# Kernel optimization log

Measured on AMD Instinct MI355X. Metric: run time of the kernel, lower is better.

## Reference

```python
import jax, jax.numpy as jnp
import numpy as np

MODES = 16
WIDTH = 64
INPUT_DIM = 12
N_LAYERS = 4
FACTOR = 2
B, M, N = 16, 128, 128


def _ff(x, w1, b1, w2, b2):
    # FeedForward: Linear -> ReLU -> Linear
    return jax.nn.relu(x @ w1 + b1) @ w2 + b2


def setup_inputs() -> dict:
    key = jax.random.key(0)
    ks = jax.random.split(key, 24)
    D, H = WIDTH, WIDTH * FACTOR
    # xavier-ish scale for complex fourier weights: sqrt(2/(fan_in+fan_out))
    fw_scale = float(np.sqrt(2.0 / (D + D)))
    def rn(k, shape, s=0.05):
        return (jax.random.normal(k, shape, dtype=jnp.float32) * s)
    return {
        "x": jax.random.normal(ks[0], (B, M, N, INPUT_DIM), dtype=jnp.float32),
        "in_w": rn(ks[1], (INPUT_DIM, D), 0.2),
        "in_b": jnp.zeros((D,), jnp.float32),
        "fwy_re": rn(ks[2], (N_LAYERS, D, D, MODES), fw_scale),
        "fwy_im": rn(ks[3], (N_LAYERS, D, D, MODES), fw_scale),
        "fwx_re": rn(ks[4], (N_LAYERS, D, D, MODES), fw_scale),
        "fwx_im": rn(ks[5], (N_LAYERS, D, D, MODES), fw_scale),
        "bc_w1": rn(ks[6], (N_LAYERS, D, H), 0.1),
        "bc_b1": jnp.zeros((N_LAYERS, H), jnp.float32),
        "bc_w2": rn(ks[7], (N_LAYERS, H, D), 0.1),
        "bc_b2": jnp.zeros((N_LAYERS, D), jnp.float32),
        "fc_w1": rn(ks[8], (N_LAYERS, D, H), 0.1),
        "fc_b1": jnp.zeros((N_LAYERS, H), jnp.float32),
        "fc_w2": rn(ks[9], (N_LAYERS, H, D), 0.1),
        "fc_b2": jnp.zeros((N_LAYERS, D), jnp.float32),
        "out_w1": rn(ks[10], (D, 128), 0.1),
        "out_b1": jnp.zeros((128,), jnp.float32),
        "out_w2": rn(ks[11], (128, 1), 0.1),
        "out_b2": jnp.zeros((1,), jnp.float32),
    }


def reference(x, in_w, in_b, fwy_re, fwy_im, fwx_re, fwx_im,
              bc_w1, bc_b1, bc_w2, bc_b2, fc_w1, fc_b1, fc_w2, fc_b2,
              out_w1, out_b1, out_w2, out_b2):
    fwy = (fwy_re + 1j * fwy_im).astype(jnp.complex64)  # [L, I, O, modes]
    fwx = (fwx_re + 1j * fwx_im).astype(jnp.complex64)
    x = x @ in_w + in_b  # [B, M, N, width]
    forecast = jnp.zeros(x.shape[:3] + (1,), x.dtype)
    for i in range(N_LAYERS):
        xt = jnp.transpose(x, (0, 3, 1, 2))  # b i m n
        _, _, Mm, Nn = xt.shape
        # spectral conv along last (y) axis
        fty = jnp.fft.rfft(xt, axis=-1, norm='ortho')  # [B,I,M,N//2+1]
        py = jnp.einsum('bixy,ioy->boxy', fty[..., :MODES], fwy[i])
        py = jnp.pad(py, ((0, 0), (0, 0), (0, 0), (0, Nn // 2 + 1 - MODES)))
        xy = jnp.fft.irfft(py, n=Nn, axis=-1, norm='ortho')
        # spectral conv along second-to-last (x) axis
        ftx = jnp.fft.rfft(xt, axis=-2, norm='ortho')  # [B,I,M//2+1,N]
        px = jnp.einsum('bixy,iox->boxy', ftx[:, :, :MODES, :], fwx[i])
        px = jnp.pad(px, ((0, 0), (0, 0), (0, Mm // 2 + 1 - MODES), (0, 0)))
        xx = jnp.fft.irfft(px, n=Mm, axis=-2, norm='ortho')
        xs = jnp.transpose(xx + xy, (0, 2, 3, 1))  # b m n i
        b = _ff(xs, bc_w1[i], bc_b1[i], bc_w2[i], bc_b2[i])
        f = _ff(xs, fc_w1[i], fc_b1[i], fc_w2[i], fc_b2[i])
        f_out = (f @ out_w1 + out_b1) @ out_w2 + out_b2  # [B,M,N,1]
        forecast = forecast + f_out
        x = x - b  # next_input='subtract'
    return forecast
```

## Files before the change

kernel.cpp:

```cpp
#include <hip/hip_runtime.h>

#define B_    16
#define M_    128
#define N_    128
#define DIN   12
#define D_    64
#define H_    128
#define MODES 16
#define NL    4
#define NPIX  262144

typedef float  f32x2 __attribute__((ext_vector_type(2)));
typedef float  f32x4 __attribute__((ext_vector_type(4)));
typedef short  s16x8 __attribute__((ext_vector_type(8)));
typedef unsigned int u32x4 __attribute__((ext_vector_type(4)));

#define WSB_X      0L
#define WSB_XSX    67108864L
#define WSB_BF     100663296L
#define WSB_BI     100671488L
#define WSB_U      100679680L
#define WSB_D      100681728L
#define WSB_WFF    100681744L
#define WSB_WMIX   100878352L
#define WS_NEEDED  102975504L

__device__ __forceinline__ unsigned short f2bf(float f){
    unsigned int u = __float_as_uint(f);
    u += 0x7fffu + ((u >> 16) & 1u);
    return (unsigned short)(u >> 16);
}
__device__ __forceinline__ float bf2f(unsigned short s){
    return __uint_as_float(((unsigned int)s) << 16);
}

__global__ void k_init(const float* __restrict__ out_w1, const float* __restrict__ out_b1,
                       const float* __restrict__ out_w2, const float* __restrict__ out_b2,
                       const float* __restrict__ fc_w2, const float* __restrict__ fc_b2,
                       float* __restrict__ ws){
    __shared__ float v_s[64];
    __shared__ float c_s;
    int t = threadIdx.x;
    if (t < 64){
        float a = 0.f;
        for (int j = 0; j < H_; j++) a += out_w1[t*H_ + j] * out_w2[j];
        v_s[t] = a;
    }
    if (t == 64){
        float a = 0.f;
        for (int j = 0; j < H_; j++) a += out_b1[j] * out_w2[j];
        c_s = a + out_b2[0];
    }
    __syncthreads();
    float* uw = (float*)((char*)ws + WSB_U);
    float* dw = (float*)((char*)ws + WSB_D);
    if (t < 128){
        for (int l = 0; l < NL; l++){
            float a = 0.f;
            for (int o = 0; o < D_; o++) a += fc_w2[(l*H_ + t)*D_ + o] * v_s[o];
            uw[l*128 + t] = a;
        }
    }
    if (t >= 128 && t < 132){
        int l = t - 128;
        float a = 0.f;
        for (int o = 0; o < D_; o++) a += fc_b2[l*D_ + o] * v_s[o];
        dw[l] = a + c_s;
    }
    const float isn = 0.08838834764831845f;
    unsigned short* bft = (unsigned short*)((char*)ws + WSB_BF);
    unsigned short* bit = (unsigned short*)((char*)ws + WSB_BI);
    for (int e = t; e < 4096; e += 256){
        { int kp = e >> 7, n = e & 127, k = kp >> 1;
          float ang = 6.283185307179586f * (float)((k*n) & 127) / 128.0f;
          bft[e] = f2bf((kp & 1) ? (-sinf(ang)*isn) : (cosf(ang)*isn)); }
        { int n = e >> 5, kp = e & 31, k = kp >> 1;
          float ang = 6.283185307179586f * (float)((k*n) & 127) / 128.0f;
          float val;
          if (kp & 1) val = (k == 0) ? 0.f : (-2.f*sinf(ang)*isn);
          else        val = ((k == 0) ? 1.f : 2.f) * cosf(ang) * isn;
          bit[e] = f2bf(val); }
    }
}

__global__ void k_wconv(const float* __restrict__ bc_w1, const float* __restrict__ fc_w1,
                        const float* __restrict__ bc_w2, float* __restrict__ ws){
    unsigned short* wb = (unsigned short*)((char*)ws + WSB_WFF);
    int e = blockIdx.x*256 + threadIdx.x;
    int a = e >> 15;
    int r = e & 32767;
    int l = r >> 13;
    int q = r & 8191;
    if (a == 0){
        int j = q >> 6, i = q & 63;
        wb[e] = f2bf(bc_w1[(l*D_ + i)*H_ + j]);
    } else if (a == 1){
        int j = q >> 6, i = q & 63;
        wb[e] = f2bf(fc_w1[(l*D_ + i)*H_ + j]);
    } else {
        int o = q >> 7, j = q & 127;
        wb[e] = f2bf(bc_w2[(l*H_ + j)*D_ + o]);
    }
}

__global__ void k_wmix(const float* __restrict__ fwy_re, const float* __restrict__ fwy_im,
                       const float* __restrict__ fwx_re, const float* __restrict__ fwx_im,
                       float* __restrict__ ws){
    unsigned int* wm = (unsigned int*)((char*)ws + WSB_WMIX);
    int e = blockIdx.x*256 + threadIdx.x;
    int ax = e >> 18;
    int r  = e & 262143;
    int l  = r >> 16;
    int k  = (r >> 12) & 15;
    int i  = (r >> 6) & 63;
    int o  = r & 63;
    long sidx = (((long)l*64 + i)*64 + o)*16 + k;
    float re = ax ? fwx_re[sidx] : fwy_re[sidx];
    float im = ax ? fwx_im[sidx] : fwy_im[sidx];
    wm[e] = (unsigned int)f2bf(re) | ((unsigned int)f2bf(im) << 16);
}

__global__ __launch_bounds__(256) void k_embed(const float* __restrict__ xin,
                                               const float* __restrict__ in_w,
                                               const float* __restrict__ in_b,
                                               float* __restrict__ X){
    long row = (long)blockIdx.x*4 + (threadIdx.x >> 6);
    int d = threadIdx.x & 63;
    const float* xr = xin + row*DIN;
    float acc = in_b[d];
    #pragma unroll
    for (int i = 0; i < DIN; i++) acc += xr[i] * in_w[i*D_ + d];
    X[row*D_ + d] = acc;
}

__global__ __launch_bounds__(256, 3) void k_spec_x(float* __restrict__ ws_f, int layer){
    __shared__ __attribute__((aligned(16))) char lds[49152];
    int t = threadIdx.x, w = t >> 6, lane = t & 63;
    int l15 = lane & 15, l4 = lane >> 4;
    int bb = blockIdx.x >> 6;
    int c  = blockIdx.x & 63;
    const float* X = ws_f;

    for (int s = 0; s < 2; s++){
        long base = (long)bb*1048576 + (long)(c*2 + s)*64;
        char* xst = lds + s*16384;
        #pragma unroll
        for (int it = 0; it < 4; it++){
            int iq = t & 15, np = (t >> 4) + it*16;
            int i0 = iq*4;
            f32x4 v0 = *(const f32x4*)&X[base + (long)(2*np)*8192 + i0];
            f32x4 v1 = *(const f32x4*)&X[base + (long)(2*np + 1)*8192 + i0];
            #pragma unroll
            for (int j = 0; j < 4; j++){
                int i = i0 + j;
                unsigned int pk = (unsigned int)f2bf(v0[j]) | ((unsigned int)f2bf(v1[j]) << 16);
                *(unsigned int*)(xst + i*256 + ((np*4) ^ ((i & 15) << 4))) = pk;
            }
        }
    }
    {
        const unsigned short* bfg = (const unsigned short*)((char*)ws_f + WSB_BF);
        for (int e = t; e < 512; e += 256){
            int kp = e >> 4, c16 = e & 15;
            s16x8 v = *(const s16x8*)&bfg[e*8];
            *(s16x8*)(lds + 32768 + kp*256 + ((c16*16) ^ ((kp & 7) << 4))) = v;
        }
    }
    __syncthreads();

    int mt = w & 1, nt0 = (w >> 1)*2;
    for (int s = 0; s < 2; s++){
        char* xst = lds + s*16384;
        f32x4 acc[2] = {{0.f,0.f,0.f,0.f},{0.f,0.f,0.f,0.f}};
        #pragma unroll
        for (int ks = 0; ks < 4; ks++){
            int kpr = mt*16 + l15;
            s16x8 a = *(const s16x8*)(lds + 32768 + kpr*256 + (((l4*16) + ks*64) ^ ((kpr & 7) << 4)));
            #pragma unroll
            for (int nf = 0; nf < 2; nf++){
                int i = (nt0 + nf)*16 + l15;
                s16x8 b = *(const s16x8*)(xst + i*256 + (((l4*16) + ks*64) ^ ((i & 15) << 4)));
                acc[nf] = __builtin_amdgcn_mfma_f32_16x16x32_bf16(a, b, acc[nf], 0, 0, 0);
            }
        }
        char* Ts = lds + 40960 + s*4096;
        #pragma unroll
        for (int nf = 0; nf < 2; nf++){
            int i = (nt0 + nf)*16 + l15;
            #pragma unroll
            for (int q = 0; q < 4; q++){
                int kp = mt*16 + l4*4 + q;
                *(unsigned short*)(Ts + kp*128 + ((i*2) ^ ((kp & 7) << 4))) = f2bf(acc[nf][q]);
            }
        }
    }
    __syncthreads();

    {
        const unsigned short* big = (const unsigned short*)((char*)ws_f + WSB_BI);
        for (int e = t; e < 512; e += 256){
            int n = e >> 2, k8 = e & 3;
            s16x8 v = *(const s16x8*)&big[e*8];
            *(s16x8*)(lds + n*80 + ((k8*16) ^ ((n & 3) << 4))) = v;
        }
    }
    {
        int k = t >> 4, og = t & 15;
        const unsigned int* Wg = (const unsigned int*)((char*)ws_f + WSB_WMIX)
                                 + ((long)(4 + layer)*16 + k)*4096;
        const char* T0 = lds + 40960;
        const char* T1 = lds + 45056;
        int rre = 2*k, rim = 2*k + 1;
        float pre0[4] = {0,0,0,0}, pim0[4] = {0,0,0,0};
        float pre1[4] = {0,0,0,0}, pim1[4] = {0,0,0,0};
        for (int i0 = 0; i0 < 64; i0 += 8){
            s16x8 tr0 = *(const s16x8*)(T0 + rre*128 + ((i0*2) ^ ((rre & 7) << 4)));
            s16x8 ti0 = *(const s16x8*)(T0 + rim*128 + ((i0*2) ^ ((rim & 7) << 4)));
            s16x8 tr1 = *(const s16x8*)(T1 + rre*128 + ((i0*2) ^ ((rre & 7) << 4)));
            s16x8 ti1 = *(const s16x8*)(T1 + rim*128 + ((i0*2) ^ ((rim & 7) << 4)));
            #pragma unroll
            for (int e = 0; e < 8; e++){
                u32x4 wv = *(const u32x4*)&Wg[(i0 + e)*64 + og*4];
                float a0 = bf2f((unsigned short)tr0[e]), b0 = bf2f((unsigned short)ti0[e]);
                float a1 = bf2f((unsigned short)tr1[e]), b1 = bf2f((unsigned short)ti1[e]);
                #pragma unroll
                for (int j = 0; j < 4; j++){
                    float wre = bf2f((unsigned short)(wv[j] & 0xffffu));
                    float wim = bf2f((unsigned short)(wv[j] >> 16));
                    pre0[j] += a0*wre - b0*wim;  pim0[j] += a0*wim + b0*wre;
                    pre1[j] += a1*wre - b1*wim;  pim1[j] += a1*wim + b1*wre;
                }
            }
        }
        #pragma unroll
        for (int j = 0; j < 4; j++){
            int o = og*4 + j;
            unsigned int pk0 = (unsigned int)f2bf(pre0[j]) | ((unsigned int)f2bf(pim0[j]) << 16);
            unsigned int pk1 = (unsigned int)f2bf(pre1[j]) | ((unsigned int)f2bf(pim1[j]) << 16);
            *(unsigned int*)(lds + 10240 + o*80 + ((k*4) ^ ((o & 3) << 4))) = pk0;
            *(unsigned int*)(lds + 15360 + o*80 + ((k*4) ^ ((o & 3) << 4))) = pk1;
        }
    }
    __syncthreads();

    unsigned short* XSx = (unsigned short*)((char*)ws_f + WSB_XSX);
    for (int s = 0; s < 2; s++){
        const char* Ps = lds + 10240 + s*5120;
        int nc = c*2 + s;
        s16x8 bfr[4];
        #pragma unroll
        for (int nt = 0; nt < 4; nt++){
            int o = nt*16 + l15;
            bfr[nt] = *(const s16x8*)(Ps + o*80 + ((l4*16) ^ ((o & 3) << 4)));
        }
        f32x4 acc[2][4];
        #pragma unroll
        for (int mi = 0; mi < 2; mi++){
            int n_ = (w*2 + mi)*16 + l15;
            s16x8 a = *(const s16x8*)(lds + n_*80 + ((l4*16) ^ ((n_ & 3) << 4)));
            #pragma unroll
            for (int nt = 0; nt < 4; nt++){
                f32x4 z = {0.f,0.f,0.f,0.f};
                acc[mi][nt] = __builtin_amdgcn_mfma_f32_16x16x32_bf16(a, bfr[nt], z, 0, 0, 0);
            }
        }
        #pragma unroll
        for (int mi = 0; mi < 2; mi++)
        #pragma unroll
        for (int nt = 0; nt < 4; nt++)
        #pragma unroll
        for (int q = 0; q < 4; q++){
            int m = (w*2 + mi)*16 + l4*4 + q;
            int o = nt*16 + l15;
            XSx[(long)bb*1048576 + (long)m*8192 + nc*64 + o] = f2bf(acc[mi][nt][q]);
        }
    }
}

__global__ __launch_bounds__(256, 2) void k_spec_y_ff(
        float* __restrict__ ws_f, float* __restrict__ out,
        const float* __restrict__ bc_b1, const float* __restrict__ bc_b2,
        const float* __restrict__ fc_b1, int layer, int first){
    __shared__ __attribute__((aligned(16))) char lds[65536];
    int t = threadIdx.x, w = t >> 6, lane = t & 63;
    int l15 = lane & 15, l4 = lane >> 4;
    long slab = blockIdx.x;
    float* X = ws_f;
    long xbase = slab*8192;

    #pragma unroll
    for (int it = 0; it < 4; it++){
        int iq = t & 15, np = (t >> 4) + it*16;
        int i0 = iq*4;
        f32x4 v0 = *(const f32x4*)&X[xbase + (long)(2*np)*64 + i0];
        f32x4 v1 = *(const f32x4*)&X[xbase + (long)(2*np + 1)*64 + i0];
        #pragma unroll
        for (int j = 0; j < 4; j++){
            int i = i0 + j;
            unsigned int pk = (unsigned int)f2bf(v0[j]) | ((unsigned int)f2bf(v1[j]) << 16);
            *(unsigned int*)(lds + i*256 + ((np*4) ^ ((i & 15) << 4))) = pk;
        }
    }
    {
        const unsigned short* bfg = (const unsigned short*)((char*)ws_f + WSB_BF);
        for (int e = t; e < 512; e += 256){
            int kp = e >> 4, c16 = e & 15;
            s16x8 v = *(const s16x8*)&bfg[e*8];
            *(s16x8*)(lds + 16384 + kp*256 + ((c16*16) ^ ((kp & 7) << 4))) = v;
        }
        const unsigned short* big = (const unsigned short*)((char*)ws_f + WSB_BI);
        for (int e = t; e < 512; e += 256){
            int n = e >> 2, k8 = e & 3;
            s16x8 v = *(const s16x8*)&big[e*8];
            *(s16x8*)(lds + 36864 + n*80 + ((k8*16) ^ ((n & 3) << 4))) = v;
        }
    }
    __syncthreads();

    {
        int mt = w & 1, nt0 = (w >> 1)*2;
        f32x4 acc[2] = {{0.f,0.f,0.f,0.f},{0.f,0.f,0.f,0.f}};
        #pragma unroll
        for (int ks = 0; ks < 4; ks++){
            int kpr = mt*16 + l15;
            s16x8 a = *(const s16x8*)(lds + 16384 + kpr*256 + (((l4*16) + ks*64) ^ ((kpr & 7) << 4)));
            #pragma unroll
            for (int nf = 0; nf < 2; nf++){
                int i = (nt0 + nf)*16 + l15;
                s16x8 b = *(const s16x8*)(lds + i*256 + (((l4*16) + ks*64) ^ ((i & 15) << 4)));
                acc[nf] = __builtin_amdgcn_mfma_f32_16x16x32_bf16(a, b, acc[nf], 0, 0, 0);
            }
        }
        #pragma unroll
        for (int nf = 0; nf < 2; nf++){
            int i = (nt0 + nf)*16 + l15;
            #pragma unroll
            for (int q = 0; q < 4; q++){
                int kp = mt*16 + l4*4 + q;
                *(unsigned short*)(lds + 32768 + kp*128 + ((i*2) ^ ((kp & 7) << 4))) = f2bf(acc[nf][q]);
            }
        }
    }
    __syncthreads();

    {
        int k = t >> 4, og = t & 15;
        const unsigned int* Wg = (const unsigned int*)((char*)ws_f + WSB_WMIX)
                                 + ((long)layer*16 + k)*4096;
        const char* T0 = lds + 32768;
        int rre = 2*k, rim = 2*k + 1;
        float pre[4] = {0,0,0,0}, pim[4] = {0,0,0,0};
        for (int i0 = 0; i0 < 64; i0 += 8){
            s16x8 tr = *(const s16x8*)(T0 + rre*128 + ((i0*2) ^ ((rre & 7) << 4)));
            s16x8 ti = *(const s16x8*)(T0 + rim*128 + ((i0*2) ^ ((rim & 7) << 4)));
            #pragma unroll
            for (int e = 0; e < 8; e++){
                u32x4 wv = *(const u32x4*)&Wg[(i0 + e)*64 + og*4];
                float a0 = bf2f((unsigned short)tr[e]), b0 = bf2f((unsigned short)ti[e]);
                #pragma unroll
                for (int j = 0; j < 4; j++){
                    float wre = bf2f((unsigned short)(wv[j] & 0xffffu));
                    float wim = bf2f((unsigned short)(wv[j] >> 16));
                    pre[j] += a0*wre - b0*wim;
                    pim[j] += a0*wim + b0*wre;
                }
            }
        }
        #pragma unroll
        for (int j = 0; j < 4; j++){
            int o = og*4 + j;
            unsigned int pk = (unsigned int)f2bf(pre[j]) | ((unsigned int)f2bf(pim[j]) << 16);
            *(unsigned int*)(lds + 47104 + o*80 + ((k*4) ^ ((o & 3) << 4))) = pk;
        }
    }
    __syncthreads();

    {
        const unsigned short* XSxg = (const unsigned short*)((char*)ws_f + WSB_XSX) + slab*8192;
        s16x8 bfr[4];
        #pragma unroll
        for (int nt = 0; nt < 4; nt++){
            int o = nt*16 + l15;
            bfr[nt] = *(const s16x8*)(lds + 47104 + o*80 + ((l4*16) ^ ((o & 3) << 4)));
        }
        f32x4 acc[2][4];
        #pragma unroll
        for (int mi = 0; mi < 2; mi++){
            int n_ = (w*2 + mi)*16 + l15;
            s16x8 a = *(const s16x8*)(lds + 36864 + n_*80 + ((l4*16) ^ ((n_ & 3) << 4)));
            #pragma unroll
            for (int nt = 0; nt < 4; nt++){
                f32x4 z = {0.f,0.f,0.f,0.f};
                acc[mi][nt] = __builtin_amdgcn_mfma_f32_16x16x32_bf16(a, bfr[nt], z, 0, 0, 0);
            }
        }
        #pragma unroll
        for (int mi = 0; mi < 2; mi++)
        #pragma unroll
        for (int nt = 0; nt < 4; nt++)
        #pragma unroll
        for (int q = 0; q < 4; q++){
            int n_ = (w*2 + mi)*16 + l4*4 + q;
            int o = nt*16 + l15;
            float v = acc[mi][nt][q] + bf2f(XSxg[n_*64 + o]);
            *(unsigned short*)(lds + n_*128 + ((o*2) ^ ((n_ & 7) << 4))) = f2bf(v);
        }
    }
    const unsigned short* wb = (const unsigned short*)((char*)ws_f + WSB_WFF);
    {
        const u32x4* src = (const u32x4*)(wb + (long)layer*8192);
        for (int cq = t; cq < 1024; cq += 256){
            int r = cq >> 3, c8 = cq & 7;
            *(u32x4*)(lds + 16384 + r*128 + ((c8 << 4) ^ ((r & 7) << 4))) = src[cq];
        }
    }
    __syncthreads();

    {
        f32x4 acc[2][8];
        #pragma unroll
        for (int mi = 0; mi < 2; mi++)
        #pragma unroll
        for (int nf = 0; nf < 8; nf++) acc[mi][nf] = (f32x4){0.f,0.f,0.f,0.f};
        #pragma unroll
        for (int ks = 0; ks < 2; ks++){
            int kch = l4 + ks*4;
            int r0 = w*32 + l15, r1 = w*32 + 16 + l15;
            s16x8 a0 = *(const s16x8*)(lds + r0*128 + ((kch << 4) ^ ((r0 & 7) << 4)));
            s16x8 a1 = *(const s16x8*)(lds + r1*128 + ((kch << 4) ^ ((r1 & 7) << 4)));
            #pragma unroll
            for (int nf = 0; nf < 8; nf++){
                int n = nf*16 + l15;
                s16x8 b = *(const s16x8*)(lds + 16384 + n*128 + ((kch << 4) ^ ((n & 7) << 4)));
                acc[0][nf] = __builtin_amdgcn_mfma_f32_16x16x32_bf16(a0, b, acc[0][nf], 0, 0, 0);
                acc[1][nf] = __builtin_amdgcn_mfma_f32_16x16x32_bf16(a1, b, acc[1][nf], 0, 0, 0);
            }
        }
        #pragma unroll
        for (int mi = 0; mi < 2; mi++)
        #pragma unroll
        for (int nf = 0; nf < 8; nf++){
            int ncol = nf*16 + l15;
            float b1 = bc_b1[layer*128 + ncol];
            #pragma unroll
            for (int q = 0; q < 4; q++){
                int mrow = w*32 + mi*16 + l4*4 + q;
                float hv = fmaxf(acc[mi][nf][q] + b1, 0.f);
                *(unsigned short*)(lds + 32768 + mrow*256 + (((ncol >> 3) << 4) ^ ((mrow & 7) << 4)) + (ncol & 7)*2) = f2bf(hv);
            }
        }
    }
    __syncthreads();
    {
        const u32x4* src = (const u32x4*)(wb + 65536 + (long)layer*8192);
        for (int cq = t; cq < 1024; cq += 256){
            int r = cq >> 4, c16 = cq & 15;
            *(u32x4*)(lds + 16384 + r*256 + ((c16 << 4) ^ ((r & 7) << 4))) = src[cq];
        }
    }
    __syncthreads();
    {
        f32x4 acc[2][4];
        #pragma unroll
        for (int mi = 0; mi < 2; mi++)
        #pragma unroll
        for (int nf = 0; nf < 4; nf++) acc[mi][nf] = (f32x4){0.f,0.f,0.f,0.f};
        #pragma unroll
        for (int ks = 0; ks < 4; ks++){
            int kch = l4 + ks*4;
            int r0 = w*32 + l15, r1 = w*32 + 16 + l15;
            s16x8 a0 = *(const s16x8*)(lds + 32768 + r0*256 + ((kch << 4) ^ ((r0 & 7) << 4)));
            s16x8 a1 = *(const s16x8*)(lds + 32768 + r1*256 + ((kch << 4) ^ ((r1 & 7) << 4)));
            #pragma unroll
            for (int nf = 0; nf < 4; nf++){
                int n = nf*16 + l15;
                s16x8 b = *(const s16x8*)(lds + 16384 + n*256 + ((kch << 4) ^ ((n & 7) << 4)));
                acc[0][nf] = __builtin_amdgcn_mfma_f32_16x16x32_bf16(a0, b, acc[0][nf], 0, 0, 0);
                acc[1][nf] = __builtin_amdgcn_mfma_f32_16x16x32_bf16(a1, b, acc[1][nf], 0, 0, 0);
            }
        }
        #pragma unroll
        for (int mi = 0; mi < 2; mi++)
        #pragma unroll
        for (int nf = 0; nf < 4; nf++){
            int ncol = nf*16 + l15;
            float b2 = bc_b2[layer*64 + ncol];
            #pragma unroll
            for (int q = 0; q < 4; q++){
                int mrow = w*32 + mi*16 + l4*4 + q;
                long g = xbase + (long)mrow*64 + ncol;
                X[g] = X[g] - (acc[mi][nf][q] + b2);
            }
        }
    }
    __syncthreads();
    {
        const u32x4* src = (const u32x4*)(wb + 32768 + (long)layer*8192);
        for (int cq = t; cq < 1024; cq += 256){
            int r = cq >> 3, c8 = cq & 7;
            *(u32x4*)(lds + 16384 + r*128 + ((c8 << 4) ^ ((r & 7) << 4))) = src[cq];
        }
    }
    __syncthreads();
    {
        f32x4 acc[2][8];
        #pragma unroll
        for (int mi = 0; mi < 2; mi++)
        #pragma unroll
        for (int nf = 0; nf < 8; nf++) acc[mi][nf] = (f32x4){0.f,0.f,0.f,0.f};
        #pragma unroll
        for (int ks = 0; ks < 2; ks++){
            int kch = l4 + ks*4;
            int r0 = w*32 + l15, r1 = w*32 + 16 + l15;
            s16x8 a0 = *(const s16x8*)(lds + r0*128 + ((kch << 4) ^ ((r0 & 7) << 4)));
            s16x8 a1 = *(const s16x8*)(lds + r1*128 + ((kch << 4) ^ ((r1 & 7) << 4)));
            #pragma unroll
            for (int nf = 0; nf < 8; nf++){
                int n = nf*16 + l15;
                s16x8 b = *(const s16x8*)(lds + 16384 + n*128 + ((kch << 4) ^ ((n & 7) << 4)));
                acc[0][nf] = __builtin_amdgcn_mfma_f32_16x16x32_bf16(a0, b, acc[0][nf], 0, 0, 0);
                acc[1][nf] = __builtin_amdgcn_mfma_f32_16x16x32_bf16(a1, b, acc[1][nf], 0, 0, 0);
            }
        }
        #pragma unroll
        for (int mi = 0; mi < 2; mi++)
        #pragma unroll
        for (int nf = 0; nf < 8; nf++){
            int ncol = nf*16 + l15;
            float b1 = fc_b1[layer*128 + ncol];
            #pragma unroll
            for (int q = 0; q < 4; q++){
                int mrow = w*32 + mi*16 + l4*4 + q;
                float hv = fmaxf(acc[mi][nf][q] + b1, 0.f);
                *(unsigned short*)(lds + 32768 + mrow*256 + (((ncol >> 3) << 4) ^ ((mrow & 7) << 4)) + (ncol & 7)*2) = f2bf(hv);
            }
        }
    }
    __syncthreads();
    {
        int r = t >> 1, half = t & 1;
        const float* up = (const float*)((char*)ws_f + WSB_U) + layer*128 + half*64;
        float sum = 0.f;
        #pragma unroll
        for (int c = 0; c < 8; c++){
            int kch = half*8 + c;
            s16x8 hv = *(const s16x8*)(lds + 32768 + r*256 + ((kch << 4) ^ ((r & 7) << 4)));
            #pragma unroll
            for (int e = 0; e < 8; e++) sum += bf2f((unsigned short)hv[e]) * up[c*8 + e];
        }
        sum += __shfl_xor(sum, 1);
        if (half == 0){
            float fo = sum + *((const float*)((char*)ws_f + WSB_D) + layer);
            long g = slab*128 + r;
            if (first) out[g] = fo; else out[g] += fo;
        }
    }
}

extern "C" void kernel_launch(void* const* d_in, const int* in_sizes, int n_in,
                              void* d_out, int out_size, void* d_ws, size_t ws_size,
                              hipStream_t stream){
    if (ws_size < (size_t)WS_NEEDED) return;
    const float* xin    = (const float*)d_in[0];
    const float* in_w   = (const float*)d_in[1];
    const float* in_b   = (const float*)d_in[2];
    const float* fwy_re = (const float*)d_in[3];
    const float* fwy_im = (const float*)d_in[4];
    const float* fwx_re = (const float*)d_in[5];
    const float* fwx_im = (const float*)d_in[6];
    const float* bc_w1  = (const float*)d_in[7];
    const float* bc_b1  = (const float*)d_in[8];
    const float* bc_w2  = (const float*)d_in[9];
    const float* bc_b2  = (const float*)d_in[10];
    const float* fc_w1  = (const float*)d_in[11];
    const float* fc_b1  = (const float*)d_in[12];
    const float* fc_w2  = (const float*)d_in[13];
    const float* fc_b2  = (const float*)d_in[14];
    const float* out_w1 = (const float*)d_in[15];
    const float* out_b1 = (const float*)d_in[16];
    const float* out_w2 = (const float*)d_in[17];
    const float* out_b2 = (const float*)d_in[18];
    float* ws  = (float*)d_ws;
    float* out = (float*)d_out;

    k_init<<<1, 256, 0, stream>>>(out_w1, out_b1, out_w2, out_b2, fc_w2, fc_b2, ws);
    k_wconv<<<384, 256, 0, stream>>>(bc_w1, fc_w1, bc_w2, ws);
    k_wmix<<<2048, 256, 0, stream>>>(fwy_re, fwy_im, fwx_re, fwx_im, ws);
    k_embed<<<NPIX/4, 256, 0, stream>>>(xin, in_w, in_b, ws);

    for (int l = 0; l < NL; l++){
        k_spec_x<<<1024, 256, 0, stream>>>(ws, l);
        k_spec_y_ff<<<2048, 256, 0, stream>>>(ws, out, bc_b1, bc_b2, fc_b1, l, l == 0 ? 1 : 0);
    }
}
```

Before: 620.2 us.

## Cut LDS footprint, keep small DFT matrices in registers, fuse final projection reduction

Both spectral kernels now load the forward and inverse DFT basis fragments straight from global memory into registers instead of staging them in LDS. The LDS buffers are reused and shrunk so more blocks fit per CU, and launch bounds are raised to match. Other changes: a packed bf16 convert instruction replaces manual rounding, the complex mode mixing is vectorized into float2 operations, and the y-FF activation fragments are kept in registers. The last fc hidden layer is reduced against the projection vector directly from MFMA accumulators with lane shuffles, removing an LDS round trip and a barrier. The trade-offs are extra global loads of small matrices, more register pressure against the higher occupancy target, and rounding that differs slightly through the packed convert.

```diff
diff --git a/kernel.cpp b/kernel.cpp
--- a/kernel.cpp
+++ b/kernel.cpp
@@ -32,6 +32,11 @@
 }
 __device__ __forceinline__ float bf2f(unsigned short s){
     return __uint_as_float(((unsigned int)s) << 16);
+}
+__device__ __forceinline__ unsigned int cvtpk(float lo, float hi){
+    unsigned int r;
+    asm("v_cvt_pk_bf16_f32 %0, %1, %2" : "=v"(r) : "v"(lo), "v"(hi));
+    return r;
 }
 
 __global__ void k_init(const float* __restrict__ out_w1, const float* __restrict__ out_b1,
@@ -133,8 +138,8 @@
     X[row*D_ + d] = acc;
 }
 
-__global__ __launch_bounds__(256, 3) void k_spec_x(float* __restrict__ ws_f, int layer){
-    __shared__ __attribute__((aligned(16))) char lds[49152];
+__global__ __launch_bounds__(256, 4) void k_spec_x(float* __restrict__ ws_f, int layer){
+    __shared__ __attribute__((aligned(16))) char lds[40960];
     int t = threadIdx.x, w = t >> 6, lane = t & 63;
     int l15 = lane & 15, l4 = lane >> 4;
     int bb = blockIdx.x >> 6;
@@ -153,66 +158,56 @@
             #pragma unroll
             for (int j = 0; j < 4; j++){
                 int i = i0 + j;
-                unsigned int pk = (unsigned int)f2bf(v0[j]) | ((unsigned int)f2bf(v1[j]) << 16);
-                *(unsigned int*)(xst + i*256 + ((np*4) ^ ((i & 15) << 4))) = pk;
-            }
-        }
-    }
+                *(unsigned int*)(xst + i*256 + ((np*4) ^ ((i & 15) << 4))) = cvtpk(v0[j], v1[j]);
+            }
+        }
+    }
+    __syncthreads();
+
+    int mt = w & 1, nt0 = (w >> 1)*2;
     {
         const unsigned short* bfg = (const unsigned short*)((char*)ws_f + WSB_BF);
-        for (int e = t; e < 512; e += 256){
-            int kp = e >> 4, c16 = e & 15;
-            s16x8 v = *(const s16x8*)&bfg[e*8];
-            *(s16x8*)(lds + 32768 + kp*256 + ((c16*16) ^ ((kp & 7) << 4))) = v;
-        }
-    }
-    __syncthreads();
-
-    int mt = w & 1, nt0 = (w >> 1)*2;
-    for (int s = 0; s < 2; s++){
-        char* xst = lds + s*16384;
-        f32x4 acc[2] = {{0.f,0.f,0.f,0.f},{0.f,0.f,0.f,0.f}};
-        #pragma unroll
-        for (int ks = 0; ks < 4; ks++){
-            int kpr = mt*16 + l15;
-            s16x8 a = *(const s16x8*)(lds + 32768 + kpr*256 + (((l4*16) + ks*64) ^ ((kpr & 7) << 4)));
+        int kpr = mt*16 + l15;
+        s16x8 bfA[4];
+        #pragma unroll
+        for (int ks = 0; ks < 4; ks++)
+            bfA[ks] = *(const s16x8*)&bfg[kpr*128 + (l4 + ks*4)*8];
+        for (int s = 0; s < 2; s++){
+            char* xst = lds + s*16384;
+            f32x4 acc[2] = {{0.f,0.f,0.f,0.f},{0.f,0.f,0.f,0.f}};
+            #pragma unroll
+            for (int ks = 0; ks < 4; ks++){
+                #pragma unroll
+                for (int nf = 0; nf < 2; nf++){
+                    int i = (nt0 + nf)*16 + l15;
+                    s16x8 b = *(const s16x8*)(xst + i*256 + (((l4*16) + ks*64) ^ ((i & 15) << 4)));
+                    acc[nf] = __builtin_amdgcn_mfma_f32_16x16x32_bf16(bfA[ks], b, acc[nf], 0, 0, 0);
+                }
+            }
+            char* Ts = lds + 32768 + s*4096;
             #pragma unroll
             for (int nf = 0; nf < 2; nf++){
                 int i = (nt0 + nf)*16 + l15;
-                s16x8 b = *(const s16x8*)(xst + i*256 + (((l4*16) + ks*64) ^ ((i & 15) << 4)));
-                acc[nf] = __builtin_amdgcn_mfma_f32_16x16x32_bf16(a, b, acc[nf], 0, 0, 0);
-            }
-        }
-        char* Ts = lds + 40960 + s*4096;
-        #pragma unroll
-        for (int nf = 0; nf < 2; nf++){
-            int i = (nt0 + nf)*16 + l15;
-            #pragma unroll
-            for (int q = 0; q < 4; q++){
-                int kp = mt*16 + l4*4 + q;
-                *(unsigned short*)(Ts + kp*128 + ((i*2) ^ ((kp & 7) << 4))) = f2bf(acc[nf][q]);
-            }
-        }
-    }
-    __syncthreads();
-
-    {
-        const unsigned short* big = (const unsigned short*)((char*)ws_f + WSB_BI);
-        for (int e = t; e < 512; e += 256){
-            int n = e >> 2, k8 = e & 3;
-            s16x8 v = *(const s16x8*)&big[e*8];
-            *(s16x8*)(lds + n*80 + ((k8*16) ^ ((n & 3) << 4))) = v;
-        }
-    }
+                #pragma unroll
+                for (int q = 0; q < 4; q++){
+                    int kp = mt*16 + l4*4 + q;
+                    *(unsigned short*)(Ts + kp*128 + ((i*2) ^ ((kp & 7) << 4))) = f2bf(acc[nf][q]);
+                }
+            }
+        }
+    }
+    __syncthreads();
+
     {
         int k = t >> 4, og = t & 15;
         const unsigned int* Wg = (const unsigned int*)((char*)ws_f + WSB_WMIX)
                                  + ((long)(4 + layer)*16 + k)*4096;
-        const char* T0 = lds + 40960;
-        const char* T1 = lds + 45056;
+        const char* T0 = lds + 32768;
+        const char* T1 = lds + 36864;
         int rre = 2*k, rim = 2*k + 1;
-        float pre0[4] = {0,0,0,0}, pim0[4] = {0,0,0,0};
-        float pre1[4] = {0,0,0,0}, pim1[4] = {0,0,0,0};
+        f32x2 p0[4], p1[4];
+        #pragma unroll
+        for (int j = 0; j < 4; j++){ p0[j] = (f32x2){0.f,0.f}; p1[j] = (f32x2){0.f,0.f}; }
         for (int i0 = 0; i0 < 64; i0 += 8){
             s16x8 tr0 = *(const s16x8*)(T0 + rre*128 + ((i0*2) ^ ((rre & 7) << 4)));
             s16x8 ti0 = *(const s16x8*)(T0 + rim*128 + ((i0*2) ^ ((rim & 7) << 4)));
@@ -221,72 +216,77 @@
             #pragma unroll
             for (int e = 0; e < 8; e++){
                 u32x4 wv = *(const u32x4*)&Wg[(i0 + e)*64 + og*4];
-                float a0 = bf2f((unsigned short)tr0[e]), b0 = bf2f((unsigned short)ti0[e]);
-                float a1 = bf2f((unsigned short)tr1[e]), b1 = bf2f((unsigned short)ti1[e]);
+                f32x2 a0 = {bf2f((unsigned short)tr0[e]), bf2f((unsigned short)tr0[e])};
+                f32x2 b0 = {bf2f((unsigned short)ti0[e]), bf2f((unsigned short)ti0[e])};
+                f32x2 a1 = {bf2f((unsigned short)tr1[e]), bf2f((unsigned short)tr1[e])};
+                f32x2 b1 = {bf2f((unsigned short)ti1[e]), bf2f((unsigned short)ti1[e])};
                 #pragma unroll
                 for (int j = 0; j < 4; j++){
-                    float wre = bf2f((unsigned short)(wv[j] & 0xffffu));
-                    float wim = bf2f((unsigned short)(wv[j] >> 16));
-                    pre0[j] += a0*wre - b0*wim;  pim0[j] += a0*wim + b0*wre;
-                    pre1[j] += a1*wre - b1*wim;  pim1[j] += a1*wim + b1*wre;
+                    float wre = __uint_as_float(wv[j] << 16);
+                    float wim = __uint_as_float(wv[j] & 0xffff0000u);
+                    f32x2 w1v = {wre, wim};
+                    f32x2 w2v = {-wim, wre};
+                    p0[j] += a0*w1v + b0*w2v;
+                    p1[j] += a1*w1v + b1*w2v;
                 }
             }
         }
         #pragma unroll
         for (int j = 0; j < 4; j++){
             int o = og*4 + j;
-            unsigned int pk0 = (unsigned int)f2bf(pre0[j]) | ((unsigned int)f2bf(pim0[j]) << 16);
-            unsigned int pk1 = (unsigned int)f2bf(pre1[j]) | ((unsigned int)f2bf(pim1[j]) << 16);
-            *(unsigned int*)(lds + 10240 + o*80 + ((k*4) ^ ((o & 3) << 4))) = pk0;
-            *(unsigned int*)(lds + 15360 + o*80 + ((k*4) ^ ((o & 3) << 4))) = pk1;
+            *(unsigned int*)(lds + o*80 + ((k*4) ^ ((o & 3) << 4)))        = cvtpk(p0[j][0], p0[j][1]);
+            *(unsigned int*)(lds + 5120 + o*80 + ((k*4) ^ ((o & 3) << 4))) = cvtpk(p1[j][0], p1[j][1]);
         }
     }
     __syncthreads();
 
     unsigned short* XSx = (unsigned short*)((char*)ws_f + WSB_XSX);
-    for (int s = 0; s < 2; s++){
-        const char* Ps = lds + 10240 + s*5120;
-        int nc = c*2 + s;
-        s16x8 bfr[4];
-        #pragma unroll
-        for (int nt = 0; nt < 4; nt++){
-            int o = nt*16 + l15;
-            bfr[nt] = *(const s16x8*)(Ps + o*80 + ((l4*16) ^ ((o & 3) << 4)));
-        }
-        f32x4 acc[2][4];
+    {
+        const unsigned short* big = (const unsigned short*)((char*)ws_f + WSB_BI);
+        s16x8 aInv[2];
         #pragma unroll
         for (int mi = 0; mi < 2; mi++){
             int n_ = (w*2 + mi)*16 + l15;
-            s16x8 a = *(const s16x8*)(lds + n_*80 + ((l4*16) ^ ((n_ & 3) << 4)));
+            aInv[mi] = *(const s16x8*)&big[n_*32 + l4*8];
+        }
+        for (int s = 0; s < 2; s++){
+            const char* Ps = lds + s*5120;
+            int nc = c*2 + s;
+            s16x8 bfr[4];
             #pragma unroll
             for (int nt = 0; nt < 4; nt++){
-                f32x4 z = {0.f,0.f,0.f,0.f};
-                acc[mi][nt] = __builtin_amdgcn_mfma_f32_16x16x32_bf16(a, bfr[nt], z, 0, 0, 0);
-            }
-        }
-        #pragma unroll
-        for (int mi = 0; mi < 2; mi++)
-        #pragma unroll
-        for (int nt = 0; nt < 4; nt++)
-        #pragma unroll
-        for (int q = 0; q < 4; q++){
-            int m = (w*2 + mi)*16 + l4*4 + q;
-            int o = nt*16 + l15;
-            XSx[(long)bb*1048576 + (long)m*8192 + nc*64 + o] = f2bf(acc[mi][nt][q]);
-        }
-    }
-}
-
-__global__ __launch_bounds__(256, 2) void k_spec_y_ff(
+                int o = nt*16 + l15;
+                bfr[nt] = *(const s16x8*)(Ps + o*80 + ((l4*16) ^ ((o & 3) << 4)));
+            }
+            #pragma unroll
+            for (int mi = 0; mi < 2; mi++){
+                #pragma unroll
+                for (int nt = 0; nt < 4; nt++){
+                    f32x4 z = {0.f,0.f,0.f,0.f};
+                    f32x4 acc = __builtin_amdgcn_mfma_f32_16x16x32_bf16(aInv[mi], bfr[nt], z, 0, 0, 0);
+                    #pragma unroll
+                    for (int q = 0; q < 4; q++){
+                        int m = (w*2 + mi)*16 + l4*4 + q;
+                        int o = nt*16 + l15;
+                        XSx[(long)bb*1048576 + (long)m*8192 + nc*64 + o] = f2bf(acc[q]);
+                    }
+                }
+            }
+        }
+    }
+}
+
+__global__ __launch_bounds__(256, 3) void k_spec_y_ff(
         float* __restrict__ ws_f, float* __restrict__ out,
         const float* __restrict__ bc_b1, const float* __restrict__ bc_b2,
         const float* __restrict__ fc_b1, int layer, int first){
-    __shared__ __attribute__((aligned(16))) char lds[65536];
+    __shared__ __attribute__((aligned(16))) char lds[49152];
     int t = threadIdx.x, w = t >> 6, lane = t & 63;
     int l15 = lane & 15, l4 = lane >> 4;
     long slab = blockIdx.x;
     float* X = ws_f;
     long xbase = slab*8192;
+    const unsigned short* wb = (const unsigned short*)((char*)ws_f + WSB_WFF);
 
     #pragma unroll
     for (int it = 0; it < 4; it++){
@@ -297,33 +297,19 @@
         #pragma unroll
         for (int j = 0; j < 4; j++){
             int i = i0 + j;
-            unsigned int pk = (unsigned int)f2bf(v0[j]) | ((unsigned int)f2bf(v1[j]) << 16);
-            *(unsigned int*)(lds + i*256 + ((np*4) ^ ((i & 15) << 4))) = pk;
-        }
-    }
+            *(unsigned int*)(lds + i*256 + ((np*4) ^ ((i & 15) << 4))) = cvtpk(v0[j], v1[j]);
+        }
+    }
+    __syncthreads();
+
+    int mt = w & 1, nt0 = (w >> 1)*2;
     {
         const unsigned short* bfg = (const unsigned short*)((char*)ws_f + WSB_BF);
-        for (int e = t; e < 512; e += 256){
-            int kp = e >> 4, c16 = e & 15;
-            s16x8 v = *(const s16x8*)&bfg[e*8];
-            *(s16x8*)(lds + 16384 + kp*256 + ((c16*16) ^ ((kp & 7) << 4))) = v;
-        }
-        const unsigned short* big = (const unsigned short*)((char*)ws_f + WSB_BI);
-        for (int e = t; e < 512; e += 256){
-            int n = e >> 2, k8 = e & 3;
-            s16x8 v = *(const s16x8*)&big[e*8];
-            *(s16x8*)(lds + 36864 + n*80 + ((k8*16) ^ ((n & 3) << 4))) = v;
-        }
-    }
-    __syncthreads();
-
-    {
-        int mt = w & 1, nt0 = (w >> 1)*2;
+        int kpr = mt*16 + l15;
         f32x4 acc[2] = {{0.f,0.f,0.f,0.f},{0.f,0.f,0.f,0.f}};
         #pragma unroll
         for (int ks = 0; ks < 4; ks++){
-            int kpr = mt*16 + l15;
-            s16x8 a = *(const s16x8*)(lds + 16384 + kpr*256 + (((l4*16) + ks*64) ^ ((kpr & 7) << 4)));
+            s16x8 a = *(const s16x8*)&bfg[kpr*128 + (l4 + ks*4)*8];
             #pragma unroll
             for (int nf = 0; nf < 2; nf++){
                 int i = (nt0 + nf)*16 + l15;
@@ -337,7 +323,7 @@
             #pragma unroll
             for (int q = 0; q < 4; q++){
                 int kp = mt*16 + l4*4 + q;
-                *(unsigned short*)(lds + 32768 + kp*128 + ((i*2) ^ ((kp & 7) << 4))) = f2bf(acc[nf][q]);
+                *(unsigned short*)(lds + 16384 + kp*128 + ((i*2) ^ ((kp & 7) << 4))) = f2bf(acc[nf][q]);
             }
         }
     }
@@ -347,71 +333,79 @@
         int k = t >> 4, og = t & 15;
         const unsigned int* Wg = (const unsigned int*)((char*)ws_f + WSB_WMIX)
                                  + ((long)layer*16 + k)*4096;
-        const char* T0 = lds + 32768;
+        const char* T0 = lds + 16384;
         int rre = 2*k, rim = 2*k + 1;
-        float pre[4] = {0,0,0,0}, pim[4] = {0,0,0,0};
+        f32x2 p[4];
+        #pragma unroll
+        for (int j = 0; j < 4; j++) p[j] = (f32x2){0.f,0.f};
         for (int i0 = 0; i0 < 64; i0 += 8){
             s16x8 tr = *(const s16x8*)(T0 + rre*128 + ((i0*2) ^ ((rre & 7) << 4)));
             s16x8 ti = *(const s16x8*)(T0 + rim*128 + ((i0*2) ^ ((rim & 7) << 4)));
             #pragma unroll
             for (int e = 0; e < 8; e++){
                 u32x4 wv = *(const u32x4*)&Wg[(i0 + e)*64 + og*4];
-                float a0 = bf2f((unsigned short)tr[e]), b0 = bf2f((unsigned short)ti[e]);
+                f32x2 av = {bf2f((unsigned short)tr[e]), bf2f((unsigned short)tr[e])};
+                f32x2 bv = {bf2f((unsigned short)ti[e]), bf2f((unsigned short)ti[e])};
                 #pragma unroll
                 for (int j = 0; j < 4; j++){
-                    float wre = bf2f((unsigned short)(wv[j] & 0xffffu));
-                    float wim = bf2f((unsigned short)(wv[j] >> 16));
-                    pre[j] += a0*wre - b0*wim;
-                    pim[j] += a0*wim + b0*wre;
+                    float wre = __uint_as_float(wv[j] << 16);
+                    float wim = __uint_as_float(wv[j] & 0xffff0000u);
+                    f32x2 w1v = {wre, wim};
+                    f32x2 w2v = {-wim, wre};
+                    p[j] += av*w1v + bv*w2v;
                 }
             }
         }
         #pragma unroll
         for (int j = 0; j < 4; j++){
             int o = og*4 + j;
-            unsigned int pk = (unsigned int)f2bf(pre[j]) | ((unsigned int)f2bf(pim[j]) << 16);
-            *(unsigned int*)(lds + 47104 + o*80 + ((k*4) ^ ((o & 3) << 4))) = pk;
-        }
-    }
-    __syncthreads();
-
-    {
+            *(unsigned int*)(lds + 20480 + o*80 + ((k*4) ^ ((o & 3) << 4))) = cvtpk(p[j][0], p[j][1]);
+        }
+    }
+    __syncthreads();
+
+    {
+        const unsigned short* big = (const unsigned short*)((char*)ws_f + WSB_BI);
         const unsigned short* XSxg = (const unsigned short*)((char*)ws_f + WSB_XSX) + slab*8192;
         s16x8 bfr[4];
         #pragma unroll
         for (int nt = 0; nt < 4; nt++){
             int o = nt*16 + l15;
-            bfr[nt] = *(const s16x8*)(lds + 47104 + o*80 + ((l4*16) ^ ((o & 3) << 4)));
-        }
-        f32x4 acc[2][4];
+            bfr[nt] = *(const s16x8*)(lds + 20480 + o*80 + ((l4*16) ^ ((o & 3) << 4)));
+        }
         #pragma unroll
         for (int mi = 0; mi < 2; mi++){
             int n_ = (w*2 + mi)*16 + l15;
-            s16x8 a = *(const s16x8*)(lds + 36864 + n_*80 + ((l4*16) ^ ((n_ & 3) << 4)));
+            s16x8 a = *(const s16x8*)&big[n_*32 + l4*8];
             #pragma unroll
             for (int nt = 0; nt < 4; nt++){
                 f32x4 z = {0.f,0.f,0.f,0.f};
-                acc[mi][nt] = __builtin_amdgcn_mfma_f32_16x16x32_bf16(a, bfr[nt], z, 0, 0, 0);
-            }
-        }
-        #pragma unroll
-        for (int mi = 0; mi < 2; mi++)
-        #pragma unroll
-        for (int nt = 0; nt < 4; nt++)
-        #pragma unroll
-        for (int q = 0; q < 4; q++){
-            int n_ = (w*2 + mi)*16 + l4*4 + q;
-            int o = nt*16 + l15;
-            float v = acc[mi][nt][q] + bf2f(XSxg[n_*64 + o]);
-            *(unsigned short*)(lds + n_*128 + ((o*2) ^ ((n_ & 7) << 4))) = f2bf(v);
-        }
-    }
-    const unsigned short* wb = (const unsigned short*)((char*)ws_f + WSB_WFF);
+                f32x4 acc = __builtin_amdgcn_mfma_f32_16x16x32_bf16(a, bfr[nt], z, 0, 0, 0);
+                #pragma unroll
+                for (int q = 0; q < 4; q++){
+                    int nr = (w*2 + mi)*16 + l4*4 + q;
+                    int o = nt*16 + l15;
+                    float v = acc[q] + bf2f(XSxg[nr*64 + o]);
+                    *(unsigned short*)(lds + 25600 + nr*128 + ((o*2) ^ ((nr & 7) << 4))) = f2bf(v);
+                }
+            }
+        }
+    }
+    __syncthreads();
+
+    s16x8 af[2][2];
+    #pragma unroll
+    for (int rr = 0; rr < 2; rr++)
+    #pragma unroll
+    for (int ks = 0; ks < 2; ks++){
+        int r = w*32 + rr*16 + l15, kch = l4 + ks*4;
+        af[rr][ks] = *(const s16x8*)(lds + 25600 + r*128 + ((kch << 4) ^ ((r & 7) << 4)));
+    }
     {
         const u32x4* src = (const u32x4*)(wb + (long)layer*8192);
         for (int cq = t; cq < 1024; cq += 256){
             int r = cq >> 3, c8 = cq & 7;
-            *(u32x4*)(lds + 16384 + r*128 + ((c8 << 4) ^ ((r & 7) << 4))) = src[cq];
+            *(u32x4*)(lds + r*128 + ((c8 << 4) ^ ((r & 7) << 4))) = src[cq];
         }
     }
     __syncthreads();
@@ -425,15 +419,12 @@
         #pragma unroll
         for (int ks = 0; ks < 2; ks++){
             int kch = l4 + ks*4;
-            int r0 = w*32 + l15, r1 = w*32 + 16 + l15;
-            s16x8 a0 = *(const s16x8*)(lds + r0*128 + ((kch << 4) ^ ((r0 & 7) << 4)));
-            s16x8 a1 = *(const s16x8*)(lds + r1*128 + ((kch << 4) ^ ((r1 & 7) << 4)));
             #pragma unroll
             for (int nf = 0; nf < 8; nf++){
                 int n = nf*16 + l15;
-                s16x8 b = *(const s16x8*)(lds + 16384 + n*128 + ((kch << 4) ^ ((n & 7) << 4)));
-                acc[0][nf] = __builtin_amdgcn_mfma_f32_16x16x32_bf16(a0, b, acc[0][nf], 0, 0, 0);
-                acc[1][nf] = __builtin_amdgcn_mfma_f32_16x16x32_bf16(a1, b, acc[1][nf], 0, 0, 0);
+                s16x8 b = *(const s16x8*)(lds + n*128 + ((kch << 4) ^ ((n & 7) << 4)));
+                acc[0][nf] = __builtin_amdgcn_mfma_f32_16x16x32_bf16(af[0][ks], b, acc[0][nf], 0, 0, 0);
+                acc[1][nf] = __builtin_amdgcn_mfma_f32_16x16x32_bf16(af[1][ks], b, acc[1][nf], 0, 0, 0);
             }
         }
         #pragma unroll
@@ -446,7 +437,7 @@
             for (int q = 0; q < 4; q++){
                 int mrow = w*32 + mi*16 + l4*4 + q;
                 float hv = fmaxf(acc[mi][nf][q] + b1, 0.f);
-                *(unsigned short*)(lds + 32768 + mrow*256 + (((ncol >> 3) << 4) ^ ((mrow & 7) << 4)) + (ncol & 7)*2) = f2bf(hv);
+                *(unsigned short*)(lds + 16384 + mrow*256 + (((ncol >> 3) << 4) ^ ((mrow & 7) << 4)) + (ncol & 7)*2) = f2bf(hv);
             }
         }
     }
@@ -455,7 +446,7 @@
         const u32x4* src = (const u32x4*)(wb + 65536 + (long)layer*8192);
         for (int cq = t; cq < 1024; cq += 256){
             int r = cq >> 4, c16 = cq & 15;
-            *(u32x4*)(lds + 16384 + r*256 + ((c16 << 4) ^ ((r & 7) << 4))) = src[cq];
+            *(u32x4*)(lds + r*256 + ((c16 << 4) ^ ((r & 7) << 4))) = src[cq];
         }
     }
     __syncthreads();
@@ -469,12 +460,12 @@
         for (int ks = 0; ks < 4; ks++){
             int kch = l4 + ks*4;
             int r0 = w*32 + l15, r1 = w*32 + 16 + l15;
-            s16x8 a0 = *(const s16x8*)(lds + 32768 + r0*256 + ((kch << 4) ^ ((r0 & 7) << 4)));
-            s16x8 a1 = *(const s16x8*)(lds + 32768 + r1*256 + ((kch << 4) ^ ((r1 & 7) << 4)));
+            s16x8 a0 = *(const s16x8*)(lds + 16384 + r0*256 + ((kch << 4) ^ ((r0 & 7) << 4)));
+            s16x8 a1 = *(const s16x8*)(lds + 16384 + r1*256 + ((kch << 4) ^ ((r1 & 7) << 4)));
             #pragma unroll
             for (int nf = 0; nf < 4; nf++){
                 int n = nf*16 + l15;
-                s16x8 b = *(const s16x8*)(lds + 16384 + n*256 + ((kch << 4) ^ ((n & 7) << 4)));
+                s16x8 b = *(const s16x8*)(lds + n*256 + ((kch << 4) ^ ((n & 7) << 4)));
                 acc[0][nf] = __builtin_amdgcn_mfma_f32_16x16x32_bf16(a0, b, acc[0][nf], 0, 0, 0);
                 acc[1][nf] = __builtin_amdgcn_mfma_f32_16x16x32_bf16(a1, b, acc[1][nf], 0, 0, 0);
             }
@@ -498,9 +489,19 @@
         const u32x4* src = (const u32x4*)(wb + 32768 + (long)layer*8192);
         for (int cq = t; cq < 1024; cq += 256){
             int r = cq >> 3, c8 = cq & 7;
-            *(u32x4*)(lds + 16384 + r*128 + ((c8 << 4) ^ ((r & 7) << 4))) = src[cq];
-        }
-    }
+            *(u32x4*)(lds + r*128 + ((c8 << 4) ^ ((r & 7) << 4))) = src[cq];
+        }
+    }
+    float uv[8], b1v[8];
+    {
+        const float* up = (const float*)((char*)ws_f + WSB_U) + layer*128;
+        #pragma unroll
+        for (int nf = 0; nf < 8; nf++){
+            uv[nf]  = up[nf*16 + l15];
+            b1v[nf] = fc_b1[layer*128 + nf*16 + l15];
+        }
+    }
+    float ddv = *((const float*)((char*)ws_f + WSB_D) + layer);
     __syncthreads();
     {
         f32x4 acc[2][8];
@@ -511,48 +512,32 @@
         #pragma unroll
         for (int ks = 0; ks < 2; ks++){
             int kch = l4 + ks*4;
-            int r0 = w*32 + l15, r1 = w*32 + 16 + l15;
-            s16x8 a0 = *(const s16x8*)(lds + r0*128 + ((kch << 4) ^ ((r0 & 7) << 4)));
-            s16x8 a1 = *(const s16x8*)(lds + r1*128 + ((kch << 4) ^ ((r1 & 7) << 4)));
             #pragma unroll
             for (int nf = 0; nf < 8; nf++){
                 int n = nf*16 + l15;
-                s16x8 b = *(const s16x8*)(lds + 16384 + n*128 + ((kch << 4) ^ ((n & 7) << 4)));
-                acc[0][nf] = __builtin_amdgcn_mfma_f32_16x16x32_bf16(a0, b, acc[0][nf], 0, 0, 0);
-                acc[1][nf] = __builtin_amdgcn_mfma_f32_16x16x32_bf16(a1, b, acc[1][nf], 0, 0, 0);
+                s16x8 b = *(const s16x8*)(lds + n*128 + ((kch << 4) ^ ((n & 7) << 4)));
+                acc[0][nf] = __builtin_amdgcn_mfma_f32_16x16x32_bf16(af[0][ks], b, acc[0][nf], 0, 0, 0);
+                acc[1][nf] = __builtin_amdgcn_mfma_f32_16x16x32_bf16(af[1][ks], b, acc[1][nf], 0, 0, 0);
             }
         }
         #pragma unroll
         for (int mi = 0; mi < 2; mi++)
         #pragma unroll
-        for (int nf = 0; nf < 8; nf++){
-            int ncol = nf*16 + l15;
-            float b1 = fc_b1[layer*128 + ncol];
-            #pragma unroll
-            for (int q = 0; q < 4; q++){
-                int mrow = w*32 + mi*16 + l4*4 + q;
-                float hv = fmaxf(acc[mi][nf][q] + b1, 0.f);
-                *(unsigned short*)(lds + 32768 + mrow*256 + (((ncol >> 3) << 4) ^ ((mrow & 7) << 4)) + (ncol & 7)*2) = f2bf(hv);
-            }
-        }
-    }
-    __syncthreads();
-    {
-        int r = t >> 1, half = t & 1;
-        const float* up = (const float*)((char*)ws_f + WSB_U) + layer*128 + half*64;
-        float sum = 0.f;
-        #pragma unroll
-        for (int c = 0; c < 8; c++){
-            int kch = half*8 + c;
-            s16x8 hv = *(const s16x8*)(lds + 32768 + r*256 + ((kch << 4) ^ ((r & 7) << 4)));
-            #pragma unroll
-            for (int e = 0; e < 8; e++) sum += bf2f((unsigned short)hv[e]) * up[c*8 + e];
-        }
-        sum += __shfl_xor(sum, 1);
-        if (half == 0){
-            float fo = sum + *((const float*)((char*)ws_f + WSB_D) + layer);
-            long g = slab*128 + r;
-            if (first) out[g] = fo; else out[g] += fo;
+        for (int q = 0; q < 4; q++){
+            float s = 0.f;
+            #pragma unroll
+            for (int nf = 0; nf < 8; nf++)
+                s += fmaxf(acc[mi][nf][q] + b1v[nf], 0.f) * uv[nf];
+            s += __shfl_xor(s, 1);
+            s += __shfl_xor(s, 2);
+            s += __shfl_xor(s, 4);
+            s += __shfl_xor(s, 8);
+            if (l15 == 0){
+                int r = w*32 + mi*16 + l4*4 + q;
+                long g = slab*128 + r;
+                float fo = s + ddv;
+                out[g] = first ? fo : (out[g] + fo);
+            }
         }
     }
 }
```

After: 680.0 us. 1.1x slower.
